# Optimization experiments

Measured on AMD Instinct MI355X. Metric: run time of the kernel, lower is better.

Reference implementation:

```python
import jax, jax.numpy as jnp
import numpy as np

N_NODES = 50000
N_EDGES = 800000
IN_CH = 128
HID_CH = 128   # 2 * out_channels
OUT_CH = 64


def setup_inputs() -> dict:
    key = jax.random.key(0)
    k1, k2, k3, k4 = jax.random.split(key, 4)
    x = jax.random.normal(k1, (N_NODES, IN_CH), dtype=jnp.float32)
    edge_index = jax.random.randint(k2, (2, N_EDGES), 0, N_NODES, dtype=jnp.int64)
    # Glorot-ish scaled weights
    W1 = jax.random.normal(k3, (IN_CH, HID_CH), dtype=jnp.float32) * (1.0 / np.sqrt(IN_CH))
    b1 = jnp.zeros((HID_CH,), dtype=jnp.float32)
    W2 = jax.random.normal(k4, (HID_CH, OUT_CH), dtype=jnp.float32) * (1.0 / np.sqrt(HID_CH))
    b2 = jnp.zeros((OUT_CH,), dtype=jnp.float32)
    return {"x": x, "edge_index": edge_index, "W1": W1, "b1": b1, "W2": W2, "b2": b2}


def _gcn_conv(x, src, dst, W, b):
    # PyG GCNConv: add self-loops, symmetric deg^-1/2 normalization,
    # linear transform, scatter-add aggregation, bias.
    n = x.shape[0]
    loop = jnp.arange(n, dtype=src.dtype)
    s = jnp.concatenate([src, loop])
    d = jnp.concatenate([dst, loop])
    ones = jnp.ones(s.shape[0], dtype=x.dtype)
    deg = jax.ops.segment_sum(ones, d, num_segments=n)  # [N]
    dinv = jnp.where(deg > 0, deg ** -0.5, 0.0)
    norm = dinv[s] * dinv[d]                             # [E+N]
    xw = x @ W                                           # [N, F_out]
    msg = xw[s] * norm[:, None]                          # gather + scale
    agg = jax.ops.segment_sum(msg, d, num_segments=n)    # scatter-add
    return agg + b


def reference(x, edge_index, W1, b1, W2, b2):
    src, dst = edge_index[0], edge_index[1]
    h = jax.nn.relu(_gcn_conv(x, src, dst, W1, b1))
    out = jax.nn.relu(_gcn_conv(h, src, dst, W2, b2))
    return out
```

## Files before the change

kernel.cpp:

```cpp
#include <hip/hip_runtime.h>
#include <hip/hip_fp16.h>

using half8 = __attribute__((ext_vector_type(8))) _Float16;
using f32x4 = __attribute__((ext_vector_type(4))) float;

#define MAXB 256
#define ECAP 5376
#define EPB  3200


__global__ void zero32(int* __restrict__ p, int n) {
    int i = blockIdx.x * 256 + threadIdx.x;
    if (i < n) p[i] = 0;
}


__global__ __launch_bounds__(256) void bin_sort(const int* __restrict__ src,
                                                const int* __restrict__ dst,
                                                int* __restrict__ bktcnt,
                                                unsigned int* __restrict__ entries,
                                                int E, int N) {
    __shared__ unsigned int ebuf[EPB];
    __shared__ unsigned char bbuf[EPB];
    __shared__ int cntL[MAXB], fillL[MAXB], baseL[MAXB];
    int tid = threadIdx.x;
    cntL[tid] = 0;
    __syncthreads();

    int e0 = blockIdx.x * EPB;
    int e1 = min(e0 + EPB, E);
    int m = e1 - e0;

    for (int i = tid; i < m; i += 256) {
        int e = e0 + i;
        int s = src[e], d = dst[e];
        int b = 0;
        unsigned int entry = 0xFFFFFFFFu;
        if ((unsigned)s < (unsigned)N && (unsigned)d < (unsigned)N) {
            b = d >> 8;
            entry = (unsigned int)s | ((unsigned int)(d & 255) << 16);
            atomicAdd(&cntL[b], 1);
        }
        ebuf[i] = entry;
        bbuf[i] = (unsigned char)b;
    }
    __syncthreads();

    int c = cntL[tid];
    if (c > 0) baseL[tid] = atomicAdd(&bktcnt[tid], c);
    fillL[tid] = 0;
    __syncthreads();

    for (int i = tid; i < m; i += 256) {
        unsigned int entry = ebuf[i];
        if (entry == 0xFFFFFFFFu) continue;
        int b = bbuf[i];
        int pos = atomicAdd(&fillL[b], 1);
        int idx = baseL[b] + pos;
        if (idx < ECAP) entries[(size_t)b * ECAP + idx] = entry;
    }
}


__global__ void scan_buckets(const int* __restrict__ bktcnt, int* __restrict__ bktbase, int nbkt) {
    __shared__ int s[256];
    int tid = threadIdx.x;
    int v = (tid < nbkt) ? min(bktcnt[tid], ECAP) : 0;
    s[tid] = v;
    __syncthreads();
    for (int off = 1; off < 256; off <<= 1) {
        int t = (tid >= off) ? s[tid - off] : 0;
        __syncthreads();
        s[tid] += t;
        __syncthreads();
    }
    if (tid < nbkt) bktbase[tid] = s[tid] - v;
}


__global__ __launch_bounds__(256) void build_csr(const unsigned int* __restrict__ entries,
                                                 const int* __restrict__ bktcnt,
                                                 const int* __restrict__ bktbase,
                                                 int* __restrict__ rowp, int* __restrict__ cnt,
                                                 float* __restrict__ dinv, int* __restrict__ col_src,
                                                 int N) {
    __shared__ int cntL[256], offL[256], fillL[256];
    int b = blockIdx.x, tid = threadIdx.x;
    cntL[tid] = 0;
    __syncthreads();

    int tot = min(bktcnt[b], ECAP);
    const unsigned int* sp = entries + (size_t)b * ECAP;
    for (int i = tid; i < tot; i += 256) atomicAdd(&cntL[(sp[i] >> 16) & 255], 1);
    __syncthreads();

    int v = cntL[tid];
    offL[tid] = v;
    __syncthreads();
    for (int off = 1; off < 256; off <<= 1) {
        int t = (tid >= off) ? offL[tid - off] : 0;
        __syncthreads();
        offL[tid] += t;
        __syncthreads();
    }

    int base = bktbase[b];
    int ex = offL[tid] - v;
    int node = (b << 8) + tid;
    if (node < N) {
        rowp[node] = base + ex;
        cnt[node]  = v;
        dinv[node] = rsqrtf((float)(v + 1));
    }
    fillL[tid] = ex;
    __syncthreads();

    for (int i = tid; i < tot; i += 256) {
        unsigned int e = sp[i];
        int slot = atomicAdd(&fillL[(e >> 16) & 255], 1);
        col_src[base + slot] = (int)(e & 0xFFFFu);
    }
}


__global__ void xd_half(const float* __restrict__ x, const float* __restrict__ dinv,
                        __half2* __restrict__ xd2, int n64) {
    int idx = blockIdx.x * 256 + threadIdx.x;
    if (idx >= n64) return;
    int row = idx >> 6;
    float di = dinv[row];
    float2 xv = *(const float2*)&x[(size_t)idx * 2];
    xd2[idx] = __float22half2_rn(make_float2(di * xv.x, di * xv.y));
}


__global__ void pack_weights(const float* __restrict__ W1, const float* __restrict__ W2,
                             _Float16* __restrict__ W1p, _Float16* __restrict__ W2p) {
    int idx = blockIdx.x * 256 + threadIdx.x;
    if (idx < 32 * 512) {
        int f = idx >> 9, rem = idx & 511, l = rem >> 3, j = rem & 7;
        int kt = f >> 3, nt = f & 7;
        int k = kt * 32 + (l >> 4) * 8 + j;
        int c = nt * 16 + (l & 15);
        W1p[idx] = (_Float16)W1[k * 128 + c];
    } else if (idx < 32 * 512 + 16 * 512) {
        int i2 = idx - 32 * 512;
        int f = i2 >> 9, rem = i2 & 511, l = rem >> 3, j = rem & 7;
        int kt = f >> 2, nt = f & 3;
        int k = kt * 32 + (l >> 4) * 8 + j;
        int c = nt * 16 + (l & 15);
        W2p[i2] = (_Float16)W2[k * 64 + c];
    }
}


__global__ void agg_x128_h(const __half2* __restrict__ x2, const int* __restrict__ rowp,
                           const int* __restrict__ cnt, const int* __restrict__ col,
                           const float* __restrict__ dinv, __half2* __restrict__ out2, int n) {
    int node = blockIdx.x * 4 + (threadIdx.x >> 6);
    if (node >= n) return;
    int lane = threadIdx.x & 63;
    float2 self = __half22float2(x2[(size_t)node * 64 + lane]);
    float ax0 = self.x, ay0 = self.y;
    float ax1 = 0.f, ay1 = 0.f, ax2 = 0.f, ay2 = 0.f, ax3 = 0.f, ay3 = 0.f;
    float ax4 = 0.f, ay4 = 0.f, ax5 = 0.f, ay5 = 0.f, ax6 = 0.f, ay6 = 0.f, ax7 = 0.f, ay7 = 0.f;
    int p = rowp[node];
    int deg = cnt[node];
    int k = 0;
    for (; k + 8 <= deg; k += 8) {
        int s0 = col[p + k + 0], s1 = col[p + k + 1], s2 = col[p + k + 2], s3 = col[p + k + 3];
        int s4 = col[p + k + 4], s5 = col[p + k + 5], s6 = col[p + k + 6], s7 = col[p + k + 7];
        float2 v0 = __half22float2(x2[(size_t)s0 * 64 + lane]);
        float2 v1 = __half22float2(x2[(size_t)s1 * 64 + lane]);
        float2 v2 = __half22float2(x2[(size_t)s2 * 64 + lane]);
        float2 v3 = __half22float2(x2[(size_t)s3 * 64 + lane]);
        float2 v4 = __half22float2(x2[(size_t)s4 * 64 + lane]);
        float2 v5 = __half22float2(x2[(size_t)s5 * 64 + lane]);
        float2 v6 = __half22float2(x2[(size_t)s6 * 64 + lane]);
        float2 v7 = __half22float2(x2[(size_t)s7 * 64 + lane]);
        ax0 += v0.x; ay0 += v0.y;  ax1 += v1.x; ay1 += v1.y;
        ax2 += v2.x; ay2 += v2.y;  ax3 += v3.x; ay3 += v3.y;
        ax4 += v4.x; ay4 += v4.y;  ax5 += v5.x; ay5 += v5.y;
        ax6 += v6.x; ay6 += v6.y;  ax7 += v7.x; ay7 += v7.y;
    }
    for (; k < deg; ++k) {
        float2 v = __half22float2(x2[(size_t)col[p + k] * 64 + lane]);
        ax0 += v.x; ay0 += v.y;
    }
    float ax = ((ax0 + ax1) + (ax2 + ax3)) + ((ax4 + ax5) + (ax6 + ax7));
    float ay = ((ay0 + ay1) + (ay2 + ay3)) + ((ay4 + ay5) + (ay6 + ay7));
    float di = dinv[node];
    out2[(size_t)node * 64 + lane] = __float22half2_rn(make_float2(di * ax, di * ay));
}


__global__ __launch_bounds__(256) void mlp_mfma(const _Float16* __restrict__ axh,
                                                const _Float16* __restrict__ W1p,
                                                const float* __restrict__ b1,
                                                const _Float16* __restrict__ W2p,
                                                const float* __restrict__ dinv,
                                                _Float16* __restrict__ yh, int M) {
    __shared__ _Float16 sh[4][16][136];
    int t = threadIdx.x;
    int w = t >> 6, l = t & 63;
    int rlo = l & 15, khi = l >> 4;
    int row0 = blockIdx.x * 64 + w * 16;

    half8 a[4];
    int arow = row0 + rlo;
    const _Float16* arp = axh + (size_t)arow * 128 + khi * 8;
#pragma unroll
    for (int kt = 0; kt < 4; ++kt) {
        half8 v = {};
        if (arow < M) v = *(const half8*)(arp + kt * 32);
        a[kt] = v;
    }

    f32x4 acc[8];
#pragma unroll
    for (int nt = 0; nt < 8; ++nt) acc[nt] = (f32x4){0.f, 0.f, 0.f, 0.f};
#pragma unroll
    for (int nt = 0; nt < 8; ++nt) {
#pragma unroll
        for (int kt = 0; kt < 4; ++kt) {
            half8 b = *(const half8*)&W1p[(size_t)((kt * 8 + nt) * 64 + l) * 8];
            acc[nt] = __builtin_amdgcn_mfma_f32_16x16x32_f16(a[kt], b, acc[nt], 0, 0, 0);
        }
    }

#pragma unroll
    for (int nt = 0; nt < 8; ++nt) {
        float bb = b1[nt * 16 + rlo];
#pragma unroll
        for (int r = 0; r < 4; ++r) {
            sh[w][khi * 4 + r][nt * 16 + rlo] = (_Float16)fmaxf(acc[nt][r] + bb, 0.f);
        }
    }
    __syncthreads();

    half8 a2[4];
#pragma unroll
    for (int kt = 0; kt < 4; ++kt)
        a2[kt] = *(const half8*)&sh[w][rlo][kt * 32 + khi * 8];

    f32x4 acc2[4];
#pragma unroll
    for (int nt = 0; nt < 4; ++nt) acc2[nt] = (f32x4){0.f, 0.f, 0.f, 0.f};
#pragma unroll
    for (int nt = 0; nt < 4; ++nt) {
#pragma unroll
        for (int kt = 0; kt < 4; ++kt) {
            half8 b = *(const half8*)&W2p[(size_t)((kt * 4 + nt) * 64 + l) * 8];
            acc2[nt] = __builtin_amdgcn_mfma_f32_16x16x32_f16(a2[kt], b, acc2[nt], 0, 0, 0);
        }
    }

#pragma unroll
    for (int r = 0; r < 4; ++r) {
        int row = row0 + khi * 4 + r;
        if (row < M) {
            float dn = dinv[row];
#pragma unroll
            for (int nt = 0; nt < 4; ++nt)
                yh[(size_t)row * 64 + nt * 16 + rlo] = (_Float16)(acc2[nt][r] * dn);
        }
    }
}


__global__ void agg_y64_h(const __half* __restrict__ y, const int* __restrict__ rowp,
                          const int* __restrict__ cnt, const int* __restrict__ col,
                          const float* __restrict__ dinv, const float* __restrict__ bias,
                          float* __restrict__ out, int n) {
    int node = blockIdx.x * 4 + (threadIdx.x >> 6);
    if (node >= n) return;
    int lane = threadIdx.x & 63;
    const __half* yc = y + lane;
    float a0 = __half2float(yc[(size_t)node * 64]);
    float a1 = 0.f, a2 = 0.f, a3 = 0.f, a4 = 0.f, a5 = 0.f, a6 = 0.f, a7 = 0.f;
    int p = rowp[node];
    int deg = cnt[node];
    int k = 0;
    for (; k + 8 <= deg; k += 8) {
        int s0 = col[p + k + 0], s1 = col[p + k + 1], s2 = col[p + k + 2], s3 = col[p + k + 3];
        int s4 = col[p + k + 4], s5 = col[p + k + 5], s6 = col[p + k + 6], s7 = col[p + k + 7];
        a0 += __half2float(yc[(size_t)s0 * 64]);
        a1 += __half2float(yc[(size_t)s1 * 64]);
        a2 += __half2float(yc[(size_t)s2 * 64]);
        a3 += __half2float(yc[(size_t)s3 * 64]);
        a4 += __half2float(yc[(size_t)s4 * 64]);
        a5 += __half2float(yc[(size_t)s5 * 64]);
        a6 += __half2float(yc[(size_t)s6 * 64]);
        a7 += __half2float(yc[(size_t)s7 * 64]);
    }
    for (; k < deg; ++k) {
        a0 += __half2float(yc[(size_t)col[p + k] * 64]);
    }
    float a = ((a0 + a1) + (a2 + a3)) + ((a4 + a5) + (a6 + a7));
    out[(size_t)node * 64 + lane] = fmaxf(bias[lane] + dinv[node] * a, 0.f);
}


extern "C" void kernel_launch(void* const* d_in, const int* in_sizes, int n_in,
                              void* d_out, int out_size, void* d_ws, size_t ws_size,
                              hipStream_t stream) {
    const float* x  = (const float*)d_in[0];
    const int*   ei = (const int*)d_in[1];
    const float* W1 = (const float*)d_in[2];
    const float* b1 = (const float*)d_in[3];
    const float* W2 = (const float*)d_in[4];
    const float* b2 = (const float*)d_in[5];
    float* out = (float*)d_out;

    const int N = in_sizes[0] / 128;
    const int E = in_sizes[1] / 2;
    const int nbkt = (N + 255) >> 8;
    const int* src = ei;
    const int* dst = ei + E;

    char* ws = (char*)d_ws;
    size_t off = 0;
    auto alloc = [&](size_t bytes) {
        void* p = ws + off;
        off += (bytes + 255) & ~(size_t)255;
        return p;
    };
    int*          bktcnt  = (int*)         alloc((size_t)MAXB * 4);
    int*          bktbase = (int*)         alloc((size_t)MAXB * 4);
    int*          rowp    = (int*)         alloc((size_t)N * 4);
    int*          cnt     = (int*)         alloc((size_t)N * 4);
    float*        dinv    = (float*)       alloc((size_t)N * 4);
    unsigned int* entries = (unsigned int*)alloc((size_t)nbkt * ECAP * 4);
    int*          col_src = (int*)         alloc((size_t)E * 4);
    __half2*      xdh     = (__half2*)     alloc((size_t)N * 128 * 2);
    __half2*      axh     = (__half2*)     alloc((size_t)N * 128 * 2);
    __half2*      yh      = (__half2*)     alloc((size_t)N * 64 * 2);
    _Float16*     W1p     = (_Float16*)    alloc((size_t)32 * 512 * 2);
    _Float16*     W2p     = (_Float16*)    alloc((size_t)16 * 512 * 2);

    const int binBlocks = (E + EPB - 1) / EPB;

    zero32<<<1, 256, 0, stream>>>(bktcnt, MAXB);
    bin_sort<<<binBlocks, 256, 0, stream>>>(src, dst, bktcnt, entries, E, N);
    scan_buckets<<<1, 256, 0, stream>>>(bktcnt, bktbase, nbkt);
    pack_weights<<<96, 256, 0, stream>>>(W1, W2, W1p, W2p);
    build_csr<<<nbkt, 256, 0, stream>>>(entries, bktcnt, bktbase, rowp, cnt, dinv, col_src, N);
    xd_half<<<(N * 64 + 255) / 256, 256, 0, stream>>>(x, dinv, xdh, N * 64);

    agg_x128_h<<<(N + 3) / 4, 256, 0, stream>>>(xdh, rowp, cnt, col_src, dinv, axh, N);
    mlp_mfma<<<(N + 63) / 64, 256, 0, stream>>>((const _Float16*)axh, W1p, b1, W2p, dinv,
                                                (_Float16*)yh, N);
    agg_y64_h<<<(N + 3) / 4, 256, 0, stream>>>((const __half*)yh, rowp, cnt, col_src, dinv, b2, out, N);
}
```

Baseline: 131.7 us.

## Merge prep kernels, fold bucket scan into CSR build, use 16-bit column indices

Folds the bucket-counter zeroing into the weight-packing kernel and moves the bucket prefix scan into every build_csr block, cutting two kernel launches. Column indices are stored as unsigned short, which halves index traffic in both aggregation kernels. The gather loops are unrolled to 16 loads per step with 8/4 tails, and output stores plus the MLP input loads are made nontemporal. Each build_csr block now redoes a small 256-element scan, and the 16-bit indices only hold for node counts up to 65535 (the old packing already truncated sources to 16 bits).

```diff
diff --git a/kernel.cpp b/kernel.cpp
--- a/kernel.cpp
+++ b/kernel.cpp
@@ -9,134 +9,12 @@
 #define EPB  3200
 
 
-__global__ void zero32(int* __restrict__ p, int n) {
-    int i = blockIdx.x * 256 + threadIdx.x;
-    if (i < n) p[i] = 0;
-}
-
-
-__global__ __launch_bounds__(256) void bin_sort(const int* __restrict__ src,
-                                                const int* __restrict__ dst,
-                                                int* __restrict__ bktcnt,
-                                                unsigned int* __restrict__ entries,
-                                                int E, int N) {
-    __shared__ unsigned int ebuf[EPB];
-    __shared__ unsigned char bbuf[EPB];
-    __shared__ int cntL[MAXB], fillL[MAXB], baseL[MAXB];
+__global__ void prep(const float* __restrict__ W1, const float* __restrict__ W2,
+                     _Float16* __restrict__ W1p, _Float16* __restrict__ W2p,
+                     int* __restrict__ bktcnt) {
     int tid = threadIdx.x;
-    cntL[tid] = 0;
-    __syncthreads();
-
-    int e0 = blockIdx.x * EPB;
-    int e1 = min(e0 + EPB, E);
-    int m = e1 - e0;
-
-    for (int i = tid; i < m; i += 256) {
-        int e = e0 + i;
-        int s = src[e], d = dst[e];
-        int b = 0;
-        unsigned int entry = 0xFFFFFFFFu;
-        if ((unsigned)s < (unsigned)N && (unsigned)d < (unsigned)N) {
-            b = d >> 8;
-            entry = (unsigned int)s | ((unsigned int)(d & 255) << 16);
-            atomicAdd(&cntL[b], 1);
-        }
-        ebuf[i] = entry;
-        bbuf[i] = (unsigned char)b;
-    }
-    __syncthreads();
-
-    int c = cntL[tid];
-    if (c > 0) baseL[tid] = atomicAdd(&bktcnt[tid], c);
-    fillL[tid] = 0;
-    __syncthreads();
-
-    for (int i = tid; i < m; i += 256) {
-        unsigned int entry = ebuf[i];
-        if (entry == 0xFFFFFFFFu) continue;
-        int b = bbuf[i];
-        int pos = atomicAdd(&fillL[b], 1);
-        int idx = baseL[b] + pos;
-        if (idx < ECAP) entries[(size_t)b * ECAP + idx] = entry;
-    }
-}
-
-
-__global__ void scan_buckets(const int* __restrict__ bktcnt, int* __restrict__ bktbase, int nbkt) {
-    __shared__ int s[256];
-    int tid = threadIdx.x;
-    int v = (tid < nbkt) ? min(bktcnt[tid], ECAP) : 0;
-    s[tid] = v;
-    __syncthreads();
-    for (int off = 1; off < 256; off <<= 1) {
-        int t = (tid >= off) ? s[tid - off] : 0;
-        __syncthreads();
-        s[tid] += t;
-        __syncthreads();
-    }
-    if (tid < nbkt) bktbase[tid] = s[tid] - v;
-}
-
-
-__global__ __launch_bounds__(256) void build_csr(const unsigned int* __restrict__ entries,
-                                                 const int* __restrict__ bktcnt,
-                                                 const int* __restrict__ bktbase,
-                                                 int* __restrict__ rowp, int* __restrict__ cnt,
-                                                 float* __restrict__ dinv, int* __restrict__ col_src,
-                                                 int N) {
-    __shared__ int cntL[256], offL[256], fillL[256];
-    int b = blockIdx.x, tid = threadIdx.x;
-    cntL[tid] = 0;
-    __syncthreads();
-
-    int tot = min(bktcnt[b], ECAP);
-    const unsigned int* sp = entries + (size_t)b * ECAP;
-    for (int i = tid; i < tot; i += 256) atomicAdd(&cntL[(sp[i] >> 16) & 255], 1);
-    __syncthreads();
-
-    int v = cntL[tid];
-    offL[tid] = v;
-    __syncthreads();
-    for (int off = 1; off < 256; off <<= 1) {
-        int t = (tid >= off) ? offL[tid - off] : 0;
-        __syncthreads();
-        offL[tid] += t;
-        __syncthreads();
-    }
-
-    int base = bktbase[b];
-    int ex = offL[tid] - v;
-    int node = (b << 8) + tid;
-    if (node < N) {
-        rowp[node] = base + ex;
-        cnt[node]  = v;
-        dinv[node] = rsqrtf((float)(v + 1));
-    }
-    fillL[tid] = ex;
-    __syncthreads();
-
-    for (int i = tid; i < tot; i += 256) {
-        unsigned int e = sp[i];
-        int slot = atomicAdd(&fillL[(e >> 16) & 255], 1);
-        col_src[base + slot] = (int)(e & 0xFFFFu);
-    }
-}
-
-
-__global__ void xd_half(const float* __restrict__ x, const float* __restrict__ dinv,
-                        __half2* __restrict__ xd2, int n64) {
-    int idx = blockIdx.x * 256 + threadIdx.x;
-    if (idx >= n64) return;
-    int row = idx >> 6;
-    float di = dinv[row];
-    float2 xv = *(const float2*)&x[(size_t)idx * 2];
-    xd2[idx] = __float22half2_rn(make_float2(di * xv.x, di * xv.y));
-}
-
-
-__global__ void pack_weights(const float* __restrict__ W1, const float* __restrict__ W2,
-                             _Float16* __restrict__ W1p, _Float16* __restrict__ W2p) {
-    int idx = blockIdx.x * 256 + threadIdx.x;
+    if (blockIdx.x == 0) bktcnt[tid] = 0;
+    int idx = blockIdx.x * 256 + tid;
     if (idx < 32 * 512) {
         int f = idx >> 9, rem = idx & 511, l = rem >> 3, j = rem & 7;
         int kt = f >> 3, nt = f & 7;
@@ -154,43 +32,176 @@
 }
 
 
+__global__ __launch_bounds__(256) void bin_sort(const int* __restrict__ src,
+                                                const int* __restrict__ dst,
+                                                int* __restrict__ bktcnt,
+                                                unsigned int* __restrict__ entries,
+                                                int E, int N) {
+    __shared__ unsigned int ebuf[EPB];
+    __shared__ unsigned char bbuf[EPB];
+    __shared__ int cntL[MAXB], fillL[MAXB], baseL[MAXB];
+    int tid = threadIdx.x;
+    cntL[tid] = 0;
+    __syncthreads();
+
+    int e0 = blockIdx.x * EPB;
+    int e1 = min(e0 + EPB, E);
+    int m = e1 - e0;
+
+    for (int i = tid; i < m; i += 256) {
+        int e = e0 + i;
+        int s = src[e], d = dst[e];
+        int b = 0;
+        unsigned int entry = 0xFFFFFFFFu;
+        if ((unsigned)s < (unsigned)N && (unsigned)d < (unsigned)N) {
+            b = d >> 8;
+            entry = (unsigned int)s | ((unsigned int)(d & 255) << 16);
+            atomicAdd(&cntL[b], 1);
+        }
+        ebuf[i] = entry;
+        bbuf[i] = (unsigned char)b;
+    }
+    __syncthreads();
+
+    int c = cntL[tid];
+    if (c > 0) baseL[tid] = atomicAdd(&bktcnt[tid], c);
+    fillL[tid] = 0;
+    __syncthreads();
+
+    for (int i = tid; i < m; i += 256) {
+        unsigned int entry = ebuf[i];
+        if (entry == 0xFFFFFFFFu) continue;
+        int b = bbuf[i];
+        int pos = atomicAdd(&fillL[b], 1);
+        int idx = baseL[b] + pos;
+        if (idx < ECAP) entries[(size_t)b * ECAP + idx] = entry;
+    }
+}
+
+
+__global__ __launch_bounds__(256) void build_csr(const unsigned int* __restrict__ entries,
+                                                 const int* __restrict__ bktcnt,
+                                                 int* __restrict__ rowp, int* __restrict__ cnt,
+                                                 float* __restrict__ dinv,
+                                                 unsigned short* __restrict__ col_src,
+                                                 int N, int nbkt) {
+    __shared__ int sb[256];
+    __shared__ int cntL[256], offL[256], fillL[256];
+    int b = blockIdx.x, tid = threadIdx.x;
+
+    int bv = (tid < nbkt) ? min(bktcnt[tid], ECAP) : 0;
+    sb[tid] = bv;
+    cntL[tid] = 0;
+    __syncthreads();
+    for (int off = 1; off < 256; off <<= 1) {
+        int t = (tid >= off) ? sb[tid - off] : 0;
+        __syncthreads();
+        sb[tid] += t;
+        __syncthreads();
+    }
+    int tot = min(bktcnt[b], ECAP);
+    int base = sb[b] - tot;
+
+    const unsigned int* sp = entries + (size_t)b * ECAP;
+    for (int i = tid; i < tot; i += 256) atomicAdd(&cntL[(sp[i] >> 16) & 255], 1);
+    __syncthreads();
+
+    int v = cntL[tid];
+    offL[tid] = v;
+    __syncthreads();
+    for (int off = 1; off < 256; off <<= 1) {
+        int t = (tid >= off) ? offL[tid - off] : 0;
+        __syncthreads();
+        offL[tid] += t;
+        __syncthreads();
+    }
+
+    int ex = offL[tid] - v;
+    int node = (b << 8) + tid;
+    if (node < N) {
+        rowp[node] = base + ex;
+        cnt[node]  = v;
+        dinv[node] = rsqrtf((float)(v + 1));
+    }
+    fillL[tid] = ex;
+    __syncthreads();
+
+    for (int i = tid; i < tot; i += 256) {
+        unsigned int e = sp[i];
+        int slot = atomicAdd(&fillL[(e >> 16) & 255], 1);
+        col_src[base + slot] = (unsigned short)(e & 0xFFFFu);
+    }
+}
+
+
+__global__ void xd_half(const float* __restrict__ x, const float* __restrict__ dinv,
+                        __half2* __restrict__ xd2, int n64) {
+    int idx = blockIdx.x * 256 + threadIdx.x;
+    if (idx >= n64) return;
+    int row = idx >> 6;
+    float di = dinv[row];
+    float2 xv = *(const float2*)&x[(size_t)idx * 2];
+    xd2[idx] = __float22half2_rn(make_float2(di * xv.x, di * xv.y));
+}
+
+
 __global__ void agg_x128_h(const __half2* __restrict__ x2, const int* __restrict__ rowp,
-                           const int* __restrict__ cnt, const int* __restrict__ col,
+                           const int* __restrict__ cnt, const unsigned short* __restrict__ col,
                            const float* __restrict__ dinv, __half2* __restrict__ out2, int n) {
     int node = blockIdx.x * 4 + (threadIdx.x >> 6);
     if (node >= n) return;
     int lane = threadIdx.x & 63;
     float2 self = __half22float2(x2[(size_t)node * 64 + lane]);
-    float ax0 = self.x, ay0 = self.y;
-    float ax1 = 0.f, ay1 = 0.f, ax2 = 0.f, ay2 = 0.f, ax3 = 0.f, ay3 = 0.f;
-    float ax4 = 0.f, ay4 = 0.f, ax5 = 0.f, ay5 = 0.f, ax6 = 0.f, ay6 = 0.f, ax7 = 0.f, ay7 = 0.f;
+    float ax[8], ay[8];
+    ax[0] = self.x; ay[0] = self.y;
+#pragma unroll
+    for (int j = 1; j < 8; ++j) { ax[j] = 0.f; ay[j] = 0.f; }
     int p = rowp[node];
     int deg = cnt[node];
     int k = 0;
-    for (; k + 8 <= deg; k += 8) {
-        int s0 = col[p + k + 0], s1 = col[p + k + 1], s2 = col[p + k + 2], s3 = col[p + k + 3];
-        int s4 = col[p + k + 4], s5 = col[p + k + 5], s6 = col[p + k + 6], s7 = col[p + k + 7];
-        float2 v0 = __half22float2(x2[(size_t)s0 * 64 + lane]);
-        float2 v1 = __half22float2(x2[(size_t)s1 * 64 + lane]);
-        float2 v2 = __half22float2(x2[(size_t)s2 * 64 + lane]);
-        float2 v3 = __half22float2(x2[(size_t)s3 * 64 + lane]);
-        float2 v4 = __half22float2(x2[(size_t)s4 * 64 + lane]);
-        float2 v5 = __half22float2(x2[(size_t)s5 * 64 + lane]);
-        float2 v6 = __half22float2(x2[(size_t)s6 * 64 + lane]);
-        float2 v7 = __half22float2(x2[(size_t)s7 * 64 + lane]);
-        ax0 += v0.x; ay0 += v0.y;  ax1 += v1.x; ay1 += v1.y;
-        ax2 += v2.x; ay2 += v2.y;  ax3 += v3.x; ay3 += v3.y;
-        ax4 += v4.x; ay4 += v4.y;  ax5 += v5.x; ay5 += v5.y;
-        ax6 += v6.x; ay6 += v6.y;  ax7 += v7.x; ay7 += v7.y;
+    for (; k + 16 <= deg; k += 16) {
+        float2 v[16];
+#pragma unroll
+        for (int j = 0; j < 16; ++j) {
+            int s = col[p + k + j];
+            v[j] = __half22float2(x2[(size_t)s * 64 + lane]);
+        }
+#pragma unroll
+        for (int j = 0; j < 16; ++j) { ax[j & 7] += v[j].x; ay[j & 7] += v[j].y; }
+    }
+    if (k + 8 <= deg) {
+        float2 v[8];
+#pragma unroll
+        for (int j = 0; j < 8; ++j) {
+            int s = col[p + k + j];
+            v[j] = __half22float2(x2[(size_t)s * 64 + lane]);
+        }
+#pragma unroll
+        for (int j = 0; j < 8; ++j) { ax[j] += v[j].x; ay[j] += v[j].y; }
+        k += 8;
+    }
+    if (k + 4 <= deg) {
+        float2 v[4];
+#pragma unroll
+        for (int j = 0; j < 4; ++j) {
+            int s = col[p + k + j];
+            v[j] = __half22float2(x2[(size_t)s * 64 + lane]);
+        }
+#pragma unroll
+        for (int j = 0; j < 4; ++j) { ax[j] += v[j].x; ay[j] += v[j].y; }
+        k += 4;
     }
     for (; k < deg; ++k) {
         float2 v = __half22float2(x2[(size_t)col[p + k] * 64 + lane]);
-        ax0 += v.x; ay0 += v.y;
-    }
-    float ax = ((ax0 + ax1) + (ax2 + ax3)) + ((ax4 + ax5) + (ax6 + ax7));
-    float ay = ((ay0 + ay1) + (ay2 + ay3)) + ((ay4 + ay5) + (ay6 + ay7));
+        ax[0] += v.x; ay[0] += v.y;
+    }
+    float axs = ((ax[0] + ax[1]) + (ax[2] + ax[3])) + ((ax[4] + ax[5]) + (ax[6] + ax[7]));
+    float ays = ((ay[0] + ay[1]) + (ay[2] + ay[3])) + ((ay[4] + ay[5]) + (ay[6] + ay[7]));
     float di = dinv[node];
-    out2[(size_t)node * 64 + lane] = __float22half2_rn(make_float2(di * ax, di * ay));
+    __half2 o = __float22half2_rn(make_float2(di * axs, di * ays));
+    unsigned int ob;
+    __builtin_memcpy(&ob, &o, 4);
+    __builtin_nontemporal_store(ob, (unsigned int*)&out2[(size_t)node * 64 + lane]);
 }
 
 
@@ -208,11 +219,11 @@
 
     half8 a[4];
     int arow = row0 + rlo;
-    const _Float16* arp = axh + (size_t)arow * 128 + khi * 8;
+    const half8* arp = (const half8*)(axh + (size_t)arow * 128 + khi * 8);
 #pragma unroll
     for (int kt = 0; kt < 4; ++kt) {
         half8 v = {};
-        if (arow < M) v = *(const half8*)(arp + kt * 32);
+        if (arow < M) v = __builtin_nontemporal_load(arp + kt * 4);
         a[kt] = v;
     }
 
@@ -269,35 +280,47 @@
 
 
 __global__ void agg_y64_h(const __half* __restrict__ y, const int* __restrict__ rowp,
-                          const int* __restrict__ cnt, const int* __restrict__ col,
+                          const int* __restrict__ cnt, const unsigned short* __restrict__ col,
                           const float* __restrict__ dinv, const float* __restrict__ bias,
                           float* __restrict__ out, int n) {
     int node = blockIdx.x * 4 + (threadIdx.x >> 6);
     if (node >= n) return;
     int lane = threadIdx.x & 63;
     const __half* yc = y + lane;
-    float a0 = __half2float(yc[(size_t)node * 64]);
-    float a1 = 0.f, a2 = 0.f, a3 = 0.f, a4 = 0.f, a5 = 0.f, a6 = 0.f, a7 = 0.f;
+    float a[8];
+    a[0] = __half2float(yc[(size_t)node * 64]);
+#pragma unroll
+    for (int j = 1; j < 8; ++j) a[j] = 0.f;
     int p = rowp[node];
     int deg = cnt[node];
     int k = 0;
-    for (; k + 8 <= deg; k += 8) {
-        int s0 = col[p + k + 0], s1 = col[p + k + 1], s2 = col[p + k + 2], s3 = col[p + k + 3];
-        int s4 = col[p + k + 4], s5 = col[p + k + 5], s6 = col[p + k + 6], s7 = col[p + k + 7];
-        a0 += __half2float(yc[(size_t)s0 * 64]);
-        a1 += __half2float(yc[(size_t)s1 * 64]);
-        a2 += __half2float(yc[(size_t)s2 * 64]);
-        a3 += __half2float(yc[(size_t)s3 * 64]);
-        a4 += __half2float(yc[(size_t)s4 * 64]);
-        a5 += __half2float(yc[(size_t)s5 * 64]);
-        a6 += __half2float(yc[(size_t)s6 * 64]);
-        a7 += __half2float(yc[(size_t)s7 * 64]);
-    }
-    for (; k < deg; ++k) {
-        a0 += __half2float(yc[(size_t)col[p + k] * 64]);
-    }
-    float a = ((a0 + a1) + (a2 + a3)) + ((a4 + a5) + (a6 + a7));
-    out[(size_t)node * 64 + lane] = fmaxf(bias[lane] + dinv[node] * a, 0.f);
+    for (; k + 16 <= deg; k += 16) {
+        float v[16];
+#pragma unroll
+        for (int j = 0; j < 16; ++j) v[j] = __half2float(yc[(size_t)col[p + k + j] * 64]);
+#pragma unroll
+        for (int j = 0; j < 16; ++j) a[j & 7] += v[j];
+    }
+    if (k + 8 <= deg) {
+        float v[8];
+#pragma unroll
+        for (int j = 0; j < 8; ++j) v[j] = __half2float(yc[(size_t)col[p + k + j] * 64]);
+#pragma unroll
+        for (int j = 0; j < 8; ++j) a[j] += v[j];
+        k += 8;
+    }
+    if (k + 4 <= deg) {
+        float v[4];
+#pragma unroll
+        for (int j = 0; j < 4; ++j) v[j] = __half2float(yc[(size_t)col[p + k + j] * 64]);
+#pragma unroll
+        for (int j = 0; j < 4; ++j) a[j] += v[j];
+        k += 4;
+    }
+    for (; k < deg; ++k) a[0] += __half2float(yc[(size_t)col[p + k] * 64]);
+    float as = ((a[0] + a[1]) + (a[2] + a[3])) + ((a[4] + a[5]) + (a[6] + a[7]));
+    float o = fmaxf(bias[lane] + dinv[node] * as, 0.f);
+    __builtin_nontemporal_store(o, &out[(size_t)node * 64 + lane]);
 }
 
 
@@ -325,26 +348,23 @@
         off += (bytes + 255) & ~(size_t)255;
         return p;
     };
-    int*          bktcnt  = (int*)         alloc((size_t)MAXB * 4);
-    int*          bktbase = (int*)         alloc((size_t)MAXB * 4);
-    int*          rowp    = (int*)         alloc((size_t)N * 4);
-    int*          cnt     = (int*)         alloc((size_t)N * 4);
-    float*        dinv    = (float*)       alloc((size_t)N * 4);
-    unsigned int* entries = (unsigned int*)alloc((size_t)nbkt * ECAP * 4);
-    int*          col_src = (int*)         alloc((size_t)E * 4);
-    __half2*      xdh     = (__half2*)     alloc((size_t)N * 128 * 2);
-    __half2*      axh     = (__half2*)     alloc((size_t)N * 128 * 2);
-    __half2*      yh      = (__half2*)     alloc((size_t)N * 64 * 2);
-    _Float16*     W1p     = (_Float16*)    alloc((size_t)32 * 512 * 2);
-    _Float16*     W2p     = (_Float16*)    alloc((size_t)16 * 512 * 2);
+    int*            bktcnt  = (int*)           alloc((size_t)MAXB * 4);
+    int*            rowp    = (int*)           alloc((size_t)N * 4);
+    int*            cnt     = (int*)           alloc((size_t)N * 4);
+    float*          dinv    = (float*)         alloc((size_t)N * 4);
+    unsigned int*   entries = (unsigned int*)  alloc((size_t)nbkt * ECAP * 4);
+    unsigned short* col_src = (unsigned short*)alloc((size_t)E * 2);
+    __half2*        xdh     = (__half2*)       alloc((size_t)N * 128 * 2);
+    __half2*        axh     = (__half2*)       alloc((size_t)N * 128 * 2);
+    __half2*        yh      = (__half2*)       alloc((size_t)N * 64 * 2);
+    _Float16*       W1p     = (_Float16*)      alloc((size_t)32 * 512 * 2);
+    _Float16*       W2p     = (_Float16*)      alloc((size_t)16 * 512 * 2);
 
     const int binBlocks = (E + EPB - 1) / EPB;
 
-    zero32<<<1, 256, 0, stream>>>(bktcnt, MAXB);
+    prep<<<96, 256, 0, stream>>>(W1, W2, W1p, W2p, bktcnt);
     bin_sort<<<binBlocks, 256, 0, stream>>>(src, dst, bktcnt, entries, E, N);
-    scan_buckets<<<1, 256, 0, stream>>>(bktcnt, bktbase, nbkt);
-    pack_weights<<<96, 256, 0, stream>>>(W1, W2, W1p, W2p);
-    build_csr<<<nbkt, 256, 0, stream>>>(entries, bktcnt, bktbase, rowp, cnt, dinv, col_src, N);
+    build_csr<<<nbkt, 256, 0, stream>>>(entries, bktcnt, rowp, cnt, dinv, col_src, N, nbkt);
     xd_half<<<(N * 64 + 255) / 256, 256, 0, stream>>>(x, dinv, xdh, N * 64);
 
     agg_x128_h<<<(N + 3) / 4, 256, 0, stream>>>(xdh, rowp, cnt, col_src, dinv, axh, N);
```

New measurement: 116.4 us. 11.6% less time.
